# Optimization experiments

Measured on AMD Instinct MI355X. Metric: run time of the kernel, lower is better.

The kernel has to match this reference:

```python
import jax, jax.numpy as jnp
import numpy as np

HQ, HKV, HD = 16, 4, 64  # q heads, kv heads, head dim
ROPE_BASE = 10000.0


def _rope_tables(n, dim):
    inv_freq = 1.0 / (ROPE_BASE ** (jnp.arange(0, dim, 2, dtype=jnp.float32) / dim))
    t = jnp.arange(n, dtype=jnp.float32)
    freqs = jnp.outer(t, inv_freq)           # [N, dim/2]
    emb = jnp.concatenate([freqs, freqs], -1)  # [N, dim]
    return jnp.cos(emb), jnp.sin(emb)


def _rotate_half(x):
    h = x.shape[-1] // 2
    return jnp.concatenate([-x[..., h:], x[..., :h]], axis=-1)


def _apply_rope(x, cos, sin):
    # x: [B, N, H, D]; cos/sin: [N, D]
    c = cos[None, :, None, :]
    s = sin[None, :, None, :]
    return x * c + _rotate_half(x) * s


def setup_inputs() -> dict:
    key = jax.random.key(0)
    ks = jax.random.split(key, 5)
    B, N, D = 2, 4096, 1024
    kvD = HKV * HD
    sc = 0.02
    return {
        "x": jax.random.normal(ks[0], (B, N, D), jnp.float32),
        "Wq": jax.random.normal(ks[1], (D, D), jnp.float32) * sc,
        "Wk": jax.random.normal(ks[2], (D, kvD), jnp.float32) * sc,
        "Wv": jax.random.normal(ks[3], (D, kvD), jnp.float32) * sc,
        "Wo": jax.random.normal(ks[4], (D, D), jnp.float32) * sc,
    }


def reference(x, Wq, Wk, Wv, Wo):
    B, N, D = x.shape
    G = HQ // HKV
    Q = (x @ Wq).reshape(B, N, HQ, HD)
    K = (x @ Wk).reshape(B, N, HKV, HD)
    V = (x @ Wv).reshape(B, N, HKV, HD)

    cos, sin = _rope_tables(N, HD)
    Q = _apply_rope(Q, cos, sin)
    K = _apply_rope(K, cos, sin)

    # GQA: expand KV heads to match Q heads (repeat_interleave over head dim)
    K = jnp.repeat(K, G, axis=2)  # [B, N, HQ, HD]
    V = jnp.repeat(V, G, axis=2)

    Q = Q.transpose(0, 2, 1, 3)  # [B, HQ, N, HD]
    K = K.transpose(0, 2, 1, 3)
    V = V.transpose(0, 2, 1, 3)

    scores = jnp.einsum('bhqd,bhkd->bhqk', Q, K) / jnp.sqrt(jnp.float32(HD))
    attn = jax.nn.softmax(scores, axis=-1)
    out = jnp.einsum('bhqk,bhkd->bhqd', attn, V)  # [B, HQ, N, HD]
    out = out.transpose(0, 2, 1, 3).reshape(B, N, D)
    return out @ Wo
```

## Files before the change

### kernel.cpp

```cpp
#include <hip/hip_runtime.h>

#define HQn   16
#define HKVn  4
#define HDn   64
#define SEQN  4096
#define NB    2
#define DM    1024
#define KVD   256
#define NPACK 1536

#define QSCALE 0.18033688011112042f

typedef __attribute__((ext_vector_type(8))) short short8;
typedef __attribute__((ext_vector_type(4))) float f32x4;

#define MFMA16 __builtin_amdgcn_mfma_f32_16x16x32_bf16
#define EXP2F(x) __builtin_amdgcn_exp2f(x)

static __device__ __forceinline__ unsigned short f2bf(float f){
  union { float f; unsigned int u; } c; c.f = f;
  unsigned int r = c.u + 0x7fffu + ((c.u >> 16) & 1u);
  return (unsigned short)(r >> 16);
}

#if __has_builtin(__builtin_amdgcn_cvt_pk_bf16_f32)
typedef __attribute__((ext_vector_type(2))) __bf16 bf16x2v;
static __device__ __forceinline__ unsigned int pk_bf2(float a, float b){
  union { bf16x2v v; unsigned int u; } c;
  c.v = __builtin_amdgcn_cvt_pk_bf16_f32(a, b);
  return c.u;
}
#else
static __device__ __forceinline__ unsigned int pk_bf2(float a, float b){
  union { float f; unsigned int u; } ca, cb; ca.f = a; cb.f = b;
  return ((ca.u + 0x8000u) >> 16) | ((cb.u + 0x8000u) & 0xFFFF0000u);
}
#endif

static __device__ __forceinline__ void swap32pair(unsigned a, unsigned b, int lane,
                                                  unsigned &o0, unsigned &o1){
#if __has_builtin(__builtin_amdgcn_permlane32_swap)
  auto r = __builtin_amdgcn_permlane32_swap(a, b, false, false);
  o0 = r[0]; o1 = r[1];
#else
  int ax = ((lane ^ 32) & 63) * 4;
  unsigned as = __builtin_amdgcn_ds_bpermute(ax, a);
  unsigned bs = __builtin_amdgcn_ds_bpermute(ax, b);
  o0 = (lane < 32) ? a  : bs;
  o1 = (lane < 32) ? as : b;
#endif
}
static __device__ __forceinline__ void swap16pair(unsigned x, unsigned y, int lane,
                                                  unsigned &o0, unsigned &o1){
#if __has_builtin(__builtin_amdgcn_permlane16_swap)
  auto r = __builtin_amdgcn_permlane16_swap(x, y, false, false);
  o0 = r[0]; o1 = r[1];
#else
  int ax = ((lane ^ 16) & 63) * 4;
  unsigned xs = __builtin_amdgcn_ds_bpermute(ax, x);
  unsigned ys = __builtin_amdgcn_ds_bpermute(ax, y);
  bool odd = (lane >> 4) & 1;
  o0 = odd ? ys : x;
  o1 = odd ? y  : xs;
#endif
}

static __device__ __forceinline__ void gl2lds16(const void* g, void* l){
  __builtin_amdgcn_global_load_lds(
      (const __attribute__((address_space(1))) void*)g,
      (__attribute__((address_space(3))) void*)l, 16, 0, 0);
}

__global__ void rope_tables_k(float* __restrict__ ct, float* __restrict__ st){
  int t = blockIdx.x, d = threadIdx.x;
  int i = d & 31;
  float inv = 1.0f / powf(10000.0f, (float)i * (1.0f/32.0f));
  float ang = (float)t * inv;
  ct[t*HDn + d] = cosf(ang);
  st[t*HDn + d] = sinf(ang);
}

__global__ __launch_bounds__(256) void castx_k(const float* __restrict__ x,
                                               unsigned short* __restrict__ xb){
  size_t i = ((size_t)blockIdx.x * 256 + threadIdx.x) * 8;
  float4 a = *(const float4*)(x + i);
  float4 b = *(const float4*)(x + i + 4);
  short8 o;
  o[0]=f2bf(a.x); o[1]=f2bf(a.y); o[2]=f2bf(a.z); o[3]=f2bf(a.w);
  o[4]=f2bf(b.x); o[5]=f2bf(b.y); o[6]=f2bf(b.z); o[7]=f2bf(b.w);
  *(short8*)(xb + i) = o;
}

__global__ __launch_bounds__(256) void castw_k(
    const float* __restrict__ Wq, const float* __restrict__ Wk,
    const float* __restrict__ Wv, const float* __restrict__ Wo,
    unsigned short* __restrict__ Wqkv_t, unsigned short* __restrict__ Wot)
{
  const int z = blockIdx.z;
  const float* W; unsigned short* D; int srcN, nOff;
  if      (z == 0) { W = Wq; D = Wqkv_t; srcN = DM;  nOff = 0;    }
  else if (z == 1) { W = Wo; D = Wot;    srcN = DM;  nOff = 0;    }
  else if (z == 2) { W = Wk; D = Wqkv_t; srcN = KVD; nOff = 1024; }
  else             { W = Wv; D = Wqkv_t; srcN = KVD; nOff = 1280; }
  const int n0 = blockIdx.y * 64;
  if (n0 >= srcN) return;
  const int k0 = blockIdx.x * 64;
  const int tid = threadIdx.x;

  __shared__ float tile[64][65];
  const int lr = tid >> 4, lc = (tid & 15) * 4;
  #pragma unroll
  for (int p = 0; p < 4; p++) {
    float4 v = *(const float4*)&W[(size_t)(k0 + lr + p*16) * srcN + n0 + lc];
    tile[lr + p*16][lc+0] = v.x; tile[lr + p*16][lc+1] = v.y;
    tile[lr + p*16][lc+2] = v.z; tile[lr + p*16][lc+3] = v.w;
  }
  __syncthreads();

  const int nn = tid >> 2, kc = (tid & 3) * 16;
  unsigned short* dp = D + (size_t)(nOff + n0 + nn) * DM + k0 + kc;
  #pragma unroll
  for (int q = 0; q < 4; q++) {
    ushort4 o;
    o.x = f2bf(tile[kc + q*4 + 0][nn]);
    o.y = f2bf(tile[kc + q*4 + 1][nn]);
    o.z = f2bf(tile[kc + q*4 + 2][nn]);
    o.w = f2bf(tile[kc + q*4 + 3][nn]);
    *(ushort4*)(dp + q*4) = o;
  }
}

__global__ __launch_bounds__(256) void qkv2_k(
    const unsigned short* __restrict__ A, const unsigned short* __restrict__ Bt,
    const float* __restrict__ ct, const float* __restrict__ st,
    unsigned short* __restrict__ Qo, unsigned short* __restrict__ Ko,
    unsigned short* __restrict__ Vo)
{
  __shared__ __align__(16) short As[128][32];
  __shared__ __align__(16) short Bs[128][32];

  const int m0 = blockIdx.x * 128, n0 = blockIdx.y * 128;
  const int tid = threadIdx.x, lane = tid & 63, w = tid >> 6;
  const int wm = w >> 1, wn = w & 1;
  const int ln = lane & 15, quad = lane >> 4;

  f32x4 acc[4][4];
  #pragma unroll
  for (int i = 0; i < 4; i++)
    #pragma unroll
    for (int j = 0; j < 4; j++) acc[i][j] = (f32x4){0.f,0.f,0.f,0.f};

  const int r0 = tid >> 2, c8 = (tid & 3) * 8;
  const int r1 = r0 + 64;

  for (int k0 = 0; k0 < DM; k0 += 32) {
    gl2lds16(A  + (size_t)(m0 + r0)*DM + k0 + c8, &As[r0][c8]);
    gl2lds16(A  + (size_t)(m0 + r1)*DM + k0 + c8, &As[r1][c8]);
    gl2lds16(Bt + (size_t)(n0 + r0)*DM + k0 + c8, &Bs[r0][c8]);
    gl2lds16(Bt + (size_t)(n0 + r1)*DM + k0 + c8, &Bs[r1][c8]);
    __syncthreads();

    short8 af[4], bf[4];
    #pragma unroll
    for (int mb = 0; mb < 4; mb++) af[mb] = *(const short8*)&As[wm*64 + mb*16 + ln][quad*8];
    #pragma unroll
    for (int nb = 0; nb < 4; nb++) bf[nb] = *(const short8*)&Bs[wn*64 + nb*16 + ln][quad*8];
    #pragma unroll
    for (int mb = 0; mb < 4; mb++)
      #pragma unroll
      for (int nb = 0; nb < 4; nb++)
        acc[mb][nb] = MFMA16(af[mb], bf[nb], acc[mb][nb], 0, 0, 0);
    __syncthreads();
  }

  const int nc = n0 + wn*64;
  int kind, head;
  if (nc < 1024)      { kind = 0; head = nc >> 6;          }
  else if (nc < 1280) { kind = 1; head = (nc - 1024) >> 6; }
  else                { kind = 2; head = (nc - 1280) >> 6; }

  if (kind == 2) {
    #pragma unroll
    for (int mb = 0; mb < 4; mb++) {
      const int m = m0 + wm*64 + mb*16 + quad*4;
      const int t = m & (SEQN-1), b = m >> 12;
      #pragma unroll
      for (int nb = 0; nb < 4; nb++) {
        int d = nb*16 + ln;
        ushort4 pk;
        pk.x = f2bf(acc[mb][nb][0]); pk.y = f2bf(acc[mb][nb][1]);
        pk.z = f2bf(acc[mb][nb][2]); pk.w = f2bf(acc[mb][nb][3]);
        *(ushort4*)&Vo[(((size_t)(b*HKVn + head))*HDn + d)*SEQN + t] = pk;
      }
    }
  } else {
    #pragma unroll
    for (int mb = 0; mb < 4; mb++) {
      #pragma unroll
      for (int nb = 0; nb < 4; nb++) {
        #pragma unroll
        for (int r = 0; r < 4; r++) {
          int m = m0 + wm*64 + mb*16 + quad*4 + r;
          int t = m & (SEQN-1), b = m >> 12;
          int d = nb*16 + ln;
          float v = acc[mb][nb][r];
          float partner = (nb < 2) ? -acc[mb][nb+2][r] : acc[mb][nb-2][r];
          float cv = ct[t*HDn + d], sv = st[t*HDn + d];
          float o = v*cv + partner*sv;
          if (kind == 0) Qo[(((size_t)(b*HQn  + head))*SEQN + t)*HDn + d] = f2bf(o * QSCALE);
          else           Ko[(((size_t)(b*HKVn + head))*SEQN + t)*HDn + d] = f2bf(o);
        }
      }
    }
  }
}

__global__ __launch_bounds__(256, 4) void attn_k(
    const unsigned short* __restrict__ Q, const unsigned short* __restrict__ K,
    const unsigned short* __restrict__ Vt, unsigned short* __restrict__ AO)
{
  __shared__ __align__(16) short kb[2][64][64];
  __shared__ __align__(16) short vb[2][64][64];

  const int id  = blockIdx.x;
  const int bhv = id & 7;
  const int b   = bhv >> 2, hv = bhv & 3;
  const int rem = id >> 3;
  const int qt  = rem & 31;
  const int h   = hv*4 + (rem >> 5);
  const int q0  = qt * 128;

  const int tid = threadIdx.x, lane = tid & 63, w = tid >> 6;
  const int ln = lane & 15, quad = lane >> 4;

  const unsigned short* Qp = Q + (((size_t)(b*HQn + h))*SEQN + q0 + w*32) * HDn;
  const unsigned short* Kp = K + ((size_t)(b*HKVn + hv))*SEQN * HDn;
  const unsigned short* Vp = Vt + ((size_t)(b*HKVn + hv))*HDn * SEQN;

  short8 qf[2][2];
  qf[0][0] = *(const short8*)(Qp + ln*HDn + quad*8);
  qf[0][1] = *(const short8*)(Qp + ln*HDn + 32 + quad*8);
  qf[1][0] = *(const short8*)(Qp + (16+ln)*HDn + quad*8);
  qf[1][1] = *(const short8*)(Qp + (16+ln)*HDn + 32 + quad*8);

  short8 ones;
  #pragma unroll
  for (int j = 0; j < 8; j++) ones[j] = (short)0x3F80;

  f32x4 o[2][4], lacc[2];
  #pragma unroll
  for (int g = 0; g < 2; g++) {
    #pragma unroll
    for (int i = 0; i < 4; i++) o[g][i] = (f32x4){0.f,0.f,0.f,0.f};
    lacc[g] = (f32x4){0.f,0.f,0.f,0.f};
  }

  const int w2   = w & 1;
  const int lrow = lane >> 3;
  const int slin = lane & 7;
  const int sK   = slin ^ lrow;

  int kkey[4]; size_t vrow[4];
  #pragma unroll
  for (int i = 0; i < 4; i++) {
    const int row = w2*32 + i*8 + lrow;
    kkey[i] = 4*(row & 15) + (row >> 4);
    vrow[i] = (size_t)row * SEQN;
  }

  #define STAGE(cn, kts)                                                     \
    do {                                                                     \
      if (w < 2) {                                                           \
        _Pragma("unroll")                                                    \
        for (int i = 0; i < 4; i++)                                          \
          gl2lds16(Kp + (size_t)((kts) + kkey[i])*HDn + sK*8,                \
                   &kb[cn][w2*32 + i*8][0]);                                 \
      } else {                                                               \
        _Pragma("unroll")                                                    \
        for (int i = 0; i < 4; i++)                                          \
          gl2lds16(Vp + vrow[i] + (kts) + sK*8,                              \
                   &vb[cn][w2*32 + i*8][0]);                                 \
      }                                                                      \
    } while (0)

  const int swz0 = (( quad      ^ (ln & 7)) * 8);
  const int swz1 = (((quad + 4) ^ (ln & 7)) * 8);

  STAGE(0, 0);
  __syncthreads();

  int c = 0;
  for (int kt = 0; kt < SEQN; kt += 64) {
    if (kt + 64 < SEQN) STAGE(c ^ 1, kt + 64);

    f32x4 s[2][4];
    #pragma unroll
    for (int nb = 0; nb < 4; nb++) {
      short8 k0 = *(const short8*)&kb[c][nb*16 + ln][swz0];
      short8 k1 = *(const short8*)&kb[c][nb*16 + ln][swz1];
      f32x4 t0 = (f32x4){0.f,0.f,0.f,0.f};
      t0 = MFMA16(k0, qf[0][0], t0, 0, 0, 0);
      t0 = MFMA16(k1, qf[0][1], t0, 0, 0, 0);
      s[0][nb] = t0;
      f32x4 t1 = (f32x4){0.f,0.f,0.f,0.f};
      t1 = MFMA16(k0, qf[1][0], t1, 0, 0, 0);
      t1 = MFMA16(k1, qf[1][1], t1, 0, 0, 0);
      s[1][nb] = t1;
    }

    short8 pf[2][2];
    #pragma unroll
    for (int g = 0; g < 2; g++) {
      unsigned u0[4], u1[4];
      #pragma unroll
      for (int r = 0; r < 4; r++) {
        u0[r] = pk_bf2(EXP2F(s[g][0][r]), EXP2F(s[g][1][r]));
        u1[r] = pk_bf2(EXP2F(s[g][2][r]), EXP2F(s[g][3][r]));
      }
      union { short8 s8; unsigned u[4]; } f0, f1;
      #pragma unroll
      for (int rho = 0; rho < 2; rho++) {
        unsigned a0, a1, t0, t1;
        swap16pair(u0[rho], u0[rho+2], lane, a0, a1);
        swap32pair(a0, a1, lane, t0, t1);
        f0.u[2*rho+0] = t0; f1.u[2*rho+0] = t1;
        swap16pair(u1[rho], u1[rho+2], lane, a0, a1);
        swap32pair(a0, a1, lane, t0, t1);
        f0.u[2*rho+1] = t0; f1.u[2*rho+1] = t1;
      }
      pf[g][0] = f0.s8; pf[g][1] = f1.s8;
    }

    #pragma unroll
    for (int db = 0; db < 4; db++) {
      short8 v0 = *(const short8*)&vb[c][db*16 + ln][swz0];
      short8 v1 = *(const short8*)&vb[c][db*16 + ln][swz1];
      o[0][db] = MFMA16(pf[0][0], v0, o[0][db], 0, 0, 0);
      o[0][db] = MFMA16(pf[0][1], v1, o[0][db], 0, 0, 0);
      o[1][db] = MFMA16(pf[1][0], v0, o[1][db], 0, 0, 0);
      o[1][db] = MFMA16(pf[1][1], v1, o[1][db], 0, 0, 0);
    }
    lacc[0] = MFMA16(pf[0][0], ones, lacc[0], 0, 0, 0);
    lacc[0] = MFMA16(pf[0][1], ones, lacc[0], 0, 0, 0);
    lacc[1] = MFMA16(pf[1][0], ones, lacc[1], 0, 0, 0);
    lacc[1] = MFMA16(pf[1][1], ones, lacc[1], 0, 0, 0);

    __syncthreads();
    c ^= 1;
  }
  #undef STAGE

  #pragma unroll
  for (int g = 0; g < 2; g++) {
    float inv[4];
    #pragma unroll
    for (int r = 0; r < 4; r++) inv[r] = 1.0f / lacc[g][r];
    #pragma unroll
    for (int db = 0; db < 4; db++) {
      #pragma unroll
      for (int r = 0; r < 4; r++) {
        int gq = q0 + w*32 + g*16 + quad*4 + r;
        int d  = db*16 + ln;
        AO[(((size_t)(b*SEQN + gq))*HQn + h)*HDn + d] = f2bf(o[g][db][r] * inv[r]);
      }
    }
  }
}

__global__ __launch_bounds__(256) void oproj2_k(
    const unsigned short* __restrict__ A, const unsigned short* __restrict__ Bt,
    float* __restrict__ out)
{
  __shared__ __align__(16) short As[128][32];
  __shared__ __align__(16) short Bs[128][32];

  const int m0 = blockIdx.x * 128, n0 = blockIdx.y * 128;
  const int tid = threadIdx.x, lane = tid & 63, w = tid >> 6;
  const int wm = w >> 1, wn = w & 1;
  const int ln = lane & 15, quad = lane >> 4;

  f32x4 acc[4][4];
  #pragma unroll
  for (int i = 0; i < 4; i++)
    #pragma unroll
    for (int j = 0; j < 4; j++) acc[i][j] = (f32x4){0.f,0.f,0.f,0.f};

  const int r0 = tid >> 2, c8 = (tid & 3) * 8;
  const int r1 = r0 + 64;

  for (int k0 = 0; k0 < DM; k0 += 32) {
    gl2lds16(A  + (size_t)(m0 + r0)*DM + k0 + c8, &As[r0][c8]);
    gl2lds16(A  + (size_t)(m0 + r1)*DM + k0 + c8, &As[r1][c8]);
    gl2lds16(Bt + (size_t)(n0 + r0)*DM + k0 + c8, &Bs[r0][c8]);
    gl2lds16(Bt + (size_t)(n0 + r1)*DM + k0 + c8, &Bs[r1][c8]);
    __syncthreads();

    short8 af[4], bf[4];
    #pragma unroll
    for (int mb = 0; mb < 4; mb++) af[mb] = *(const short8*)&As[wm*64 + mb*16 + ln][quad*8];
    #pragma unroll
    for (int nb = 0; nb < 4; nb++) bf[nb] = *(const short8*)&Bs[wn*64 + nb*16 + ln][quad*8];
    #pragma unroll
    for (int mb = 0; mb < 4; mb++)
      #pragma unroll
      for (int nb = 0; nb < 4; nb++)
        acc[mb][nb] = MFMA16(af[mb], bf[nb], acc[mb][nb], 0, 0, 0);
    __syncthreads();
  }

  #pragma unroll
  for (int mb = 0; mb < 4; mb++) {
    #pragma unroll
    for (int nb = 0; nb < 4; nb++) {
      #pragma unroll
      for (int r = 0; r < 4; r++) {
        int m = m0 + wm*64 + mb*16 + quad*4 + r;
        int c = n0 + wn*64 + nb*16 + ln;
        out[(size_t)m*DM + c] = acc[mb][nb][r];
      }
    }
  }
}

extern "C" void kernel_launch(void* const* d_in, const int* in_sizes, int n_in,
                              void* d_out, int out_size, void* d_ws, size_t ws_size,
                              hipStream_t stream) {
  const float* x  = (const float*)d_in[0];
  const float* Wq = (const float*)d_in[1];
  const float* Wk = (const float*)d_in[2];
  const float* Wv = (const float*)d_in[3];
  const float* Wo = (const float*)d_in[4];
  float* out = (float*)d_out;

  char* ws = (char*)d_ws;
  float* cos_t = (float*)ws;
  float* sin_t = cos_t + SEQN*HDn;
  unsigned short* xb     = (unsigned short*)(sin_t + SEQN*HDn);
  unsigned short* AO     = xb;
  unsigned short* Wqkv_t = xb + (size_t)NB*SEQN*DM;
  unsigned short* Wot    = Wqkv_t + (size_t)NPACK*DM;
  unsigned short* Qb     = Wot + (size_t)DM*DM;
  unsigned short* Kb     = Qb + (size_t)NB*HQn *SEQN*HDn;
  unsigned short* Vb     = Kb + (size_t)NB*HKVn*SEQN*HDn;

  hipLaunchKernelGGL(rope_tables_k, dim3(SEQN), dim3(HDn), 0, stream, cos_t, sin_t);
  hipLaunchKernelGGL(castx_k, dim3((NB*SEQN*DM)/(256*8)), dim3(256), 0, stream, x, xb);
  hipLaunchKernelGGL(castw_k, dim3(16, 16, 4), dim3(256), 0, stream,
                     Wq, Wk, Wv, Wo, Wqkv_t, Wot);
  hipLaunchKernelGGL(qkv2_k, dim3(64, 12), dim3(256), 0, stream,
                     xb, Wqkv_t, cos_t, sin_t, Qb, Kb, Vb);
  hipLaunchKernelGGL(attn_k, dim3(1024), dim3(256), 0, stream,
                     Qb, Kb, Vb, AO);
  hipLaunchKernelGGL(oproj2_k, dim3(64, 8), dim3(256), 0, stream,
                     AO, Wot, out);
}
```

Before: 324.5 us.

## Permute K staging rows to drop cross-lane P shuffles; add MFMA priority hints

Changes the order in which K rows are staged into LDS so the MFMA score output already lands in the register layout needed as the A operand of the PV MFMA. This removes the permlane16/permlane32 swap sequence that rebuilt P fragments every key tile. It also wraps the QK and PV MFMA blocks in s_setprio raises so waves issuing matrix ops get scheduling priority over the waves doing exp and pack work. The approach depends on the key permutation matching between score columns and V rows; a mismatch would silently give wrong results.

Result: faster. 314.9 us (-3.0%).

```diff
diff --git a/kernel.cpp b/kernel.cpp
--- a/kernel.cpp
+++ b/kernel.cpp
@@ -36,34 +36,6 @@
   return ((ca.u + 0x8000u) >> 16) | ((cb.u + 0x8000u) & 0xFFFF0000u);
 }
 #endif
-
-static __device__ __forceinline__ void swap32pair(unsigned a, unsigned b, int lane,
-                                                  unsigned &o0, unsigned &o1){
-#if __has_builtin(__builtin_amdgcn_permlane32_swap)
-  auto r = __builtin_amdgcn_permlane32_swap(a, b, false, false);
-  o0 = r[0]; o1 = r[1];
-#else
-  int ax = ((lane ^ 32) & 63) * 4;
-  unsigned as = __builtin_amdgcn_ds_bpermute(ax, a);
-  unsigned bs = __builtin_amdgcn_ds_bpermute(ax, b);
-  o0 = (lane < 32) ? a  : bs;
-  o1 = (lane < 32) ? as : b;
-#endif
-}
-static __device__ __forceinline__ void swap16pair(unsigned x, unsigned y, int lane,
-                                                  unsigned &o0, unsigned &o1){
-#if __has_builtin(__builtin_amdgcn_permlane16_swap)
-  auto r = __builtin_amdgcn_permlane16_swap(x, y, false, false);
-  o0 = r[0]; o1 = r[1];
-#else
-  int ax = ((lane ^ 16) & 63) * 4;
-  unsigned xs = __builtin_amdgcn_ds_bpermute(ax, x);
-  unsigned ys = __builtin_amdgcn_ds_bpermute(ax, y);
-  bool odd = (lane >> 4) & 1;
-  o0 = odd ? ys : x;
-  o1 = odd ? y  : xs;
-#endif
-}
 
 static __device__ __forceinline__ void gl2lds16(const void* g, void* l){
   __builtin_amdgcn_global_load_lds(
@@ -263,9 +235,8 @@
   int kkey[4]; size_t vrow[4];
   #pragma unroll
   for (int i = 0; i < 4; i++) {
-    const int row = w2*32 + i*8 + lrow;
-    kkey[i] = 4*(row & 15) + (row >> 4);
-    vrow[i] = (size_t)row * SEQN;
+    kkey[i] = 32*w2 + 16*(i & 1) + 8*(lrow >> 2) + 4*(i >> 1) + (lrow & 3);
+    vrow[i] = (size_t)(w2*32 + i*8 + lrow) * SEQN;
   }
 
   #define STAGE(cn, kts)                                                     \
@@ -294,6 +265,7 @@
     if (kt + 64 < SEQN) STAGE(c ^ 1, kt + 64);
 
     f32x4 s[2][4];
+    __builtin_amdgcn_s_setprio(1);
     #pragma unroll
     for (int nb = 0; nb < 4; nb++) {
       short8 k0 = *(const short8*)&kb[c][nb*16 + ln][swz0];
@@ -307,30 +279,23 @@
       t1 = MFMA16(k1, qf[1][1], t1, 0, 0, 0);
       s[1][nb] = t1;
     }
+    __builtin_amdgcn_s_setprio(0);
 
     short8 pf[2][2];
     #pragma unroll
     for (int g = 0; g < 2; g++) {
-      unsigned u0[4], u1[4];
-      #pragma unroll
-      for (int r = 0; r < 4; r++) {
-        u0[r] = pk_bf2(EXP2F(s[g][0][r]), EXP2F(s[g][1][r]));
-        u1[r] = pk_bf2(EXP2F(s[g][2][r]), EXP2F(s[g][3][r]));
+      #pragma unroll
+      for (int k2 = 0; k2 < 2; k2++) {
+        union { short8 s8; unsigned u[4]; } f;
+        f.u[0] = pk_bf2(EXP2F(s[g][2*k2  ][0]), EXP2F(s[g][2*k2  ][1]));
+        f.u[1] = pk_bf2(EXP2F(s[g][2*k2  ][2]), EXP2F(s[g][2*k2  ][3]));
+        f.u[2] = pk_bf2(EXP2F(s[g][2*k2+1][0]), EXP2F(s[g][2*k2+1][1]));
+        f.u[3] = pk_bf2(EXP2F(s[g][2*k2+1][2]), EXP2F(s[g][2*k2+1][3]));
+        pf[g][k2] = f.s8;
       }
-      union { short8 s8; unsigned u[4]; } f0, f1;
-      #pragma unroll
-      for (int rho = 0; rho < 2; rho++) {
-        unsigned a0, a1, t0, t1;
-        swap16pair(u0[rho], u0[rho+2], lane, a0, a1);
-        swap32pair(a0, a1, lane, t0, t1);
-        f0.u[2*rho+0] = t0; f1.u[2*rho+0] = t1;
-        swap16pair(u1[rho], u1[rho+2], lane, a0, a1);
-        swap32pair(a0, a1, lane, t0, t1);
-        f0.u[2*rho+1] = t0; f1.u[2*rho+1] = t1;
-      }
-      pf[g][0] = f0.s8; pf[g][1] = f1.s8;
-    }
-
+    }
+
+    __builtin_amdgcn_s_setprio(1);
     #pragma unroll
     for (int db = 0; db < 4; db++) {
       short8 v0 = *(const short8*)&vb[c][db*16 + ln][swz0];
@@ -344,6 +309,7 @@
     lacc[0] = MFMA16(pf[0][1], ones, lacc[0], 0, 0, 0);
     lacc[1] = MFMA16(pf[1][0], ones, lacc[1], 0, 0, 0);
     lacc[1] = MFMA16(pf[1][1], ones, lacc[1], 0, 0, 0);
+    __builtin_amdgcn_s_setprio(0);
 
     __syncthreads();
     c ^= 1;
```
